# Kernel optimization log

Measured on AMD Instinct MI355X. Metric: run time of the kernel, lower is better.

Reference implementation:

```python
import jax, jax.numpy as jnp
import numpy as np

N, D, H = 50000, 128, 2        # nodes, hidden_size(=ffn_size=out_channels), heads
E = 800000                      # edges
C = D                           # per-head out_channels (PyG TransformerConv)
EPS = 1e-5

def layer_norm(x, g, b):
    mu = jnp.mean(x, axis=-1, keepdims=True)
    var = jnp.mean((x - mu) ** 2, axis=-1, keepdims=True)
    return (x - mu) / jnp.sqrt(var + EPS) * g + b

def setup_inputs() -> dict:
    key = jax.random.key(0)
    ks = jax.random.split(key, 16)
    s_in = 1.0 / np.sqrt(D)
    s_ffn = 1.0 / np.sqrt(D)
    return {
        "x": jax.random.normal(ks[0], (N, D), jnp.float32),
        "edge_index": jax.random.randint(ks[1], (2, E), 0, N, jnp.int64),
        "ln1_g": jnp.ones((D,), jnp.float32),
        "ln1_b": jnp.zeros((D,), jnp.float32),
        "Wq": jax.random.normal(ks[2], (D, H * C), jnp.float32) * s_in,
        "bq": jnp.zeros((H * C,), jnp.float32),
        "Wk": jax.random.normal(ks[3], (D, H * C), jnp.float32) * s_in,
        "bk": jnp.zeros((H * C,), jnp.float32),
        "Wv": jax.random.normal(ks[4], (D, H * C), jnp.float32) * s_in,
        "bv": jnp.zeros((H * C,), jnp.float32),
        "Wskip": jax.random.normal(ks[5], (D, C), jnp.float32) * s_in,
        "bskip": jnp.zeros((C,), jnp.float32),
        "ln2_g": jnp.ones((D,), jnp.float32),
        "ln2_b": jnp.zeros((D,), jnp.float32),
        "W1": jax.random.normal(ks[6], (D, D), jnp.float32) * s_ffn,
        "b1": jnp.zeros((D,), jnp.float32),
        "W2": jax.random.normal(ks[7], (D, D), jnp.float32) * s_ffn,
        "b2": jnp.zeros((D,), jnp.float32),
    }

def reference(x, edge_index, ln1_g, ln1_b, Wq, bq, Wk, bk, Wv, bv,
              Wskip, bskip, ln2_g, ln2_b, W1, b1, W2, b2):
    src, dst = edge_index[0], edge_index[1]  # messages flow src(j) -> dst(i)
    n = x.shape[0]

    # --- self-attention block (pre-norm) ---
    y = layer_norm(x, ln1_g, ln1_b)
    q = (y @ Wq + bq).reshape(n, H, C)
    k = (y @ Wk + bk).reshape(n, H, C)
    v = (y @ Wv + bv).reshape(n, H, C)

    # per-edge attention logits [E, H]
    alpha = jnp.einsum('ehc,ehc->eh', q[dst], k[src]) / jnp.sqrt(jnp.float32(C))
    # softmax over incoming edges of each dst node
    m = jax.ops.segment_max(alpha, dst, num_segments=n)          # [N, H]
    p = jnp.exp(alpha - m[dst])                                  # [E, H]
    denom = jax.ops.segment_sum(p, dst, num_segments=n)          # [N, H]
    a = p / denom[dst]                                           # [E, H]

    attn = jax.ops.segment_sum(a[:, :, None] * v[src], dst, num_segments=n)  # [N,H,C]
    out = attn.mean(axis=1) + (y @ Wskip + bskip)  # concat=False mean + root skip
    x = x + out  # residual (dropout is identity at eval)

    # --- FFN block (pre-norm) ---
    h = layer_norm(x, ln2_g, ln2_b)
    h = jax.nn.gelu(h @ W1 + b1, approximate=False) @ W2 + b2
    return x + h
```

## Files before the change

### kernel.cpp

```cpp
#include <hip/hip_runtime.h>
#include <hip/hip_bf16.h>
#include <math.h>


typedef unsigned short u16;
using short8 = __attribute__((ext_vector_type(8))) short;
using f32x4  = __attribute__((ext_vector_type(4))) float;
using f32x2  = __attribute__((ext_vector_type(2))) float;
using u32x4  = __attribute__((ext_vector_type(4))) unsigned int;

#define EST 64

__device__ __forceinline__ float bf2f(u16 u) {
    return __uint_as_float(((unsigned int)u) << 16);
}
__device__ __forceinline__ u16 f2bf(float f) {
    __hip_bfloat16 h = __float2bfloat16(f);
    return __builtin_bit_cast(u16, h);
}
__device__ __forceinline__ float bfe(short8 v, int j) {
    return bf2f((u16)v[j]);
}
__device__ __forceinline__ void fp8x4_to_f32(int w, float* out) {
    f32x2 lo = __builtin_amdgcn_cvt_pk_f32_fp8(w, false);
    f32x2 hi = __builtin_amdgcn_cvt_pk_f32_fp8(w, true);
    out[0] = lo[0]; out[1] = lo[1]; out[2] = hi[0]; out[3] = hi[1];
}
__device__ __forceinline__ unsigned pack_fp8x4(float4 f) {
    unsigned w = 0;
    w = (unsigned)__builtin_amdgcn_cvt_pk_fp8_f32(f.x, f.y, (int)w, false);
    w = (unsigned)__builtin_amdgcn_cvt_pk_fp8_f32(f.z, f.w, (int)w, true);
    return w;
}

__global__ __launch_bounds__(256) void fused_prep_ln(
    const float* __restrict__ x, const float* __restrict__ ln1g,
    const float* __restrict__ ln1b,
    const float* __restrict__ Wq, const float* __restrict__ Wk,
    const float* __restrict__ Wv, const float* __restrict__ Ws,
    const float* __restrict__ W1, const float* __restrict__ W2,
    const float* __restrict__ bq, const float* __restrict__ bk,
    const float* __restrict__ bv, const float* __restrict__ bs,
    u16* __restrict__ wt, float* __restrict__ bc,
    u16* __restrict__ y, int n)
{
    int gsz = gridDim.x * 256;
    int gtid = blockIdx.x * 256 + threadIdx.x;

    for (int i = gtid; i < 147456 + 896; i += gsz) {
        if (i < 147456) {
            const float* W; int N; int base;
            if      (i <  32768) { W = Wq; N = 256; base = 0; }
            else if (i <  65536) { W = Wk; N = 256; base = 32768; }
            else if (i <  98304) { W = Wv; N = 256; base = 65536; }
            else if (i < 114688) { W = Ws; N = 128; base = 98304; }
            else if (i < 131072) { W = W1; N = 128; base = 114688; }
            else                 { W = W2; N = 128; base = 131072; }
            int j = i - base;
            int nIdx = j >> 7, k = j & 127;
            wt[i] = f2bf(W[(size_t)k * N + nIdx]);
        } else {
            int j = i - 147456;
            float v;
            if      (j < 256) v = bq[j];
            else if (j < 512) v = bk[j - 256];
            else if (j < 768) v = bv[j - 512];
            else              v = bs[j - 768];
            bc[j] = v;
        }
    }
    int lane = threadIdx.x & 63;
    int gw = gtid >> 6, nw = gsz >> 6;
    for (int row = gw; row < n; row += nw) {
        size_t base = (size_t)row * 128;
        float v0 = x[base + lane];
        float v1 = x[base + 64 + lane];
        float s1 = v0 + v1, s2 = v0 * v0 + v1 * v1;
        for (int o = 1; o <= 32; o <<= 1) {
            s1 += __shfl_xor(s1, o);
            s2 += __shfl_xor(s2, o);
        }
        float mu = s1 * (1.f / 128.f);
        float var = s2 * (1.f / 128.f) - mu * mu;
        float rstd = rsqrtf(var + 1e-5f);
        y[base + lane]      = f2bf((v0 - mu) * rstd * ln1g[lane] + ln1b[lane]);
        y[base + 64 + lane] = f2bf((v1 - mu) * rstd * ln1g[64 + lane] + ln1b[64 + lane]);
    }
}

__global__ __launch_bounds__(256, 6) void qkv_gemm(
    const u16* __restrict__ A, const u16* __restrict__ Bt,
    const float* __restrict__ bias, u16* __restrict__ qbuf,
    unsigned char* __restrict__ kv,
    float* __restrict__ skip, int n,
    const int* __restrict__ edst, const int* __restrict__ esrcIn,
    int* __restrict__ cnt, u16* __restrict__ ebuk, int e, int scatBlocks)
{
    __shared__ float epi[4][32 * 33];
    __shared__ uint2 kst[4][2][32][4];
    if (blockIdx.x < (unsigned)scatBlocks) {
        int stride = scatBlocks * 256;
        for (int i = blockIdx.x * 256 + threadIdx.x; i < e; i += stride) {
            int d = edst[i];
            int r = atomicAdd(&cnt[d], 1);
            if (r < EST) ebuk[(size_t)d * EST + r] = (u16)esrcIn[i];
        }
        return;
    }
    int bid = blockIdx.x - scatBlocks;
    int wc = threadIdx.x >> 6, lane = threadIdx.x & 63;
    int r0 = bid * 32;
    int lm = lane & 15, quad = lane >> 4;

    int ar0 = r0 + lm;       if (ar0 > n - 1) ar0 = n - 1;
    int ar1 = r0 + 16 + lm;  if (ar1 > n - 1) ar1 = n - 1;
    const u16* aB0 = A + (size_t)ar0 * 128 + quad * 8;
    const u16* aB1 = A + (size_t)ar1 * 128 + quad * 8;
    short8 a0_0 = *(const short8*)(aB0 + 0);
    short8 a0_1 = *(const short8*)(aB0 + 32);
    short8 a0_2 = *(const short8*)(aB0 + 64);
    short8 a0_3 = *(const short8*)(aB0 + 96);
    short8 a1_0 = *(const short8*)(aB1 + 0);
    short8 a1_1 = *(const short8*)(aB1 + 32);
    short8 a1_2 = *(const short8*)(aB1 + 64);
    short8 a1_3 = *(const short8*)(aB1 + 96);
    asm volatile("" : "+v"(a0_0), "+v"(a0_1), "+v"(a0_2), "+v"(a0_3),
                      "+v"(a1_0), "+v"(a1_1), "+v"(a1_2), "+v"(a1_3));

    float* ep = epi[wc];

    for (int by = 0; by < 7; ++by) {
        int c0 = by * 128;
        const u16* bBase = Bt + (size_t)(c0 + wc * 32 + lm) * 128 + quad * 8;
        f32x4 acc[2][2] = {};
#pragma unroll
        for (int kx = 0; kx < 4; ++kx) {
            short8 a0 = (kx == 0) ? a0_0 : (kx == 1) ? a0_1 : (kx == 2) ? a0_2 : a0_3;
            short8 a1 = (kx == 0) ? a1_0 : (kx == 1) ? a1_1 : (kx == 2) ? a1_2 : a1_3;
#pragma unroll
            for (int j = 0; j < 2; ++j) {
                short8 bj = *(const short8*)(bBase + (size_t)j * 16 * 128 + kx * 32);
                acc[0][j] = __builtin_amdgcn_mfma_f32_16x16x32_bf16(a0, bj, acc[0][j], 0, 0, 0);
                acc[1][j] = __builtin_amdgcn_mfma_f32_16x16x32_bf16(a1, bj, acc[1][j], 0, 0, 0);
            }
        }
#pragma unroll
        for (int j = 0; j < 2; ++j) {
            float bv = bias[c0 + wc * 32 + j * 16 + lm];
#pragma unroll
            for (int rt = 0; rt < 2; ++rt)
#pragma unroll
                for (int i2 = 0; i2 < 4; ++i2)
                    ep[(rt * 16 + quad * 4 + i2) * 33 + j * 16 + lm]
                        = acc[rt][j][i2] + bv;
        }
        if (c0 < 256) {
            int chq = lane & 3;
#pragma unroll
            for (int it = 0; it < 2; ++it) {
                int row = it * 16 + (lane >> 2);
                int gRow = r0 + row;
                if (gRow < n) {
                    const float* ws = ep + row * 33 + chq * 8;
                    short8 o;
#pragma unroll
                    for (int jj = 0; jj < 8; ++jj) o[jj] = (short)f2bf(ws[jj]);
                    *(short8*)(qbuf + (size_t)gRow * 256 + c0 + wc * 32 + chq * 8) = o;
                }
            }
        } else if (c0 < 512) {
            int h = (c0 - 256) >> 7;
            int gp = lane & 3;
#pragma unroll
            for (int it = 0; it < 2; ++it) {
                int row = it * 16 + (lane >> 2);
                const float* ws = ep + row * 33 + gp * 8;
                uint2 kp;
                kp.x = pack_fp8x4(make_float4(ws[0], ws[1], ws[2], ws[3]));
                kp.y = pack_fp8x4(make_float4(ws[4], ws[5], ws[6], ws[7]));
                kst[wc][h][row][gp] = kp;
            }
        } else if (c0 < 768) {
            int h = (c0 - 512) >> 7;
            int gp = lane & 3;
#pragma unroll
            for (int it = 0; it < 2; ++it) {
                int row = it * 16 + (lane >> 2);
                int gRow = r0 + row;
                if (gRow < n) {
                    const float* ws = ep + row * 33 + gp * 8;
                    uint2 kp = kst[wc][h][row][gp];
                    uint4 o;
                    o.x = kp.x;
                    o.y = kp.y;
                    o.z = pack_fp8x4(make_float4(ws[0], ws[1], ws[2], ws[3]));
                    o.w = pack_fp8x4(make_float4(ws[4], ws[5], ws[6], ws[7]));
                    *(uint4*)(kv + (size_t)gRow * 512 + h * 256 + (wc * 4 + gp) * 16) = o;
                }
            }
        } else {
            int chs = lane & 7;
#pragma unroll
            for (int it = 0; it < 4; ++it) {
                int row = it * 8 + (lane >> 3);
                int gRow = r0 + row;
                if (gRow < n) {
                    const float* ws = ep + row * 33 + chs * 4;
                    *(float4*)(skip + (size_t)gRow * 128 + wc * 32 + chs * 4)
                        = make_float4(ws[0], ws[1], ws[2], ws[3]);
                }
            }
        }
    }
}

__global__ __launch_bounds__(256) void attn_kernel(
    const u16* __restrict__ qbuf, const unsigned char* __restrict__ kv,
    const int* __restrict__ cnt,
    const u16* __restrict__ ebuk, const float* __restrict__ x,
    float* __restrict__ sx, const float* __restrict__ g2,
    const float* __restrict__ b2, u16* __restrict__ y, int n, int nwaves)
{
    int wid = threadIdx.x >> 6, lane = threadIdx.x & 63;
    int gw = blockIdx.x * 4 + wid;
    int slot = lane >> 5;
    int sub  = lane & 15;
    int head = (lane >> 4) & 1;
    int colOff = head * 128 + sub * 8;
    int kvOff  = head * 256 + sub * 16;
    const float scale = 0.08838834764831845f;

    for (int i = gw; i < n; i += nwaves) {
        short8 q8 = *(const short8*)(qbuf + (size_t)i * 256 + colOff);
        float qf[8];
#pragma unroll
        for (int j = 0; j < 8; ++j) qf[j] = bfe(q8, j) * scale;

        int deg = cnt[i]; if (deg > EST) deg = EST;
        int beg = i * EST, end = beg + deg;
        float l = 0.f;
        float acc[8] = {};

        int t = beg + slot;
        for (; t + 14 < end; t += 16) {
            int ss[8];
#pragma unroll
            for (int m = 0; m < 8; ++m) ss[m] = (int)ebuk[t + 2 * m];
            u32x4 k0 = *(const u32x4*)(kv + (size_t)ss[0] * 512 + kvOff);
            u32x4 k1 = *(const u32x4*)(kv + (size_t)ss[1] * 512 + kvOff);
            u32x4 k2 = *(const u32x4*)(kv + (size_t)ss[2] * 512 + kvOff);
            u32x4 k3 = *(const u32x4*)(kv + (size_t)ss[3] * 512 + kvOff);
            u32x4 k4 = *(const u32x4*)(kv + (size_t)ss[4] * 512 + kvOff);
            u32x4 k5 = *(const u32x4*)(kv + (size_t)ss[5] * 512 + kvOff);
            u32x4 k6 = *(const u32x4*)(kv + (size_t)ss[6] * 512 + kvOff);
            u32x4 k7 = *(const u32x4*)(kv + (size_t)ss[7] * 512 + kvOff);
            asm volatile("" : "+v"(k0), "+v"(k1), "+v"(k2), "+v"(k3),
                              "+v"(k4), "+v"(k5), "+v"(k6), "+v"(k7));
            u32x4 kvv[8] = {k0, k1, k2, k3, k4, k5, k6, k7};
            float d[8];
#pragma unroll
            for (int m = 0; m < 8; ++m) {
                float kf[8];
                fp8x4_to_f32((int)kvv[m][0], kf);
                fp8x4_to_f32((int)kvv[m][1], kf + 4);
                float dm = 0.f;
#pragma unroll
                for (int j = 0; j < 8; ++j) dm += qf[j] * kf[j];
                d[m] = dm;
            }
#pragma unroll
            for (int o = 1; o <= 8; o <<= 1)
#pragma unroll
                for (int m = 0; m < 8; ++m) d[m] += __shfl_xor(d[m], o);
            float wv[8];
#pragma unroll
            for (int m = 0; m < 8; ++m) { wv[m] = __expf(d[m]); l += wv[m]; }
#pragma unroll
            for (int m = 0; m < 8; ++m) {
                float vf[8];
                fp8x4_to_f32((int)kvv[m][2], vf);
                fp8x4_to_f32((int)kvv[m][3], vf + 4);
#pragma unroll
                for (int j = 0; j < 8; ++j) acc[j] += wv[m] * vf[j];
            }
        }
        for (; t + 6 < end; t += 8) {
            int s0 = (int)ebuk[t],     s1 = (int)ebuk[t + 2];
            int s2 = (int)ebuk[t + 4], s3 = (int)ebuk[t + 6];
            u32x4 kv0 = *(const u32x4*)(kv + (size_t)s0 * 512 + kvOff);
            u32x4 kv1 = *(const u32x4*)(kv + (size_t)s1 * 512 + kvOff);
            u32x4 kv2 = *(const u32x4*)(kv + (size_t)s2 * 512 + kvOff);
            u32x4 kv3 = *(const u32x4*)(kv + (size_t)s3 * 512 + kvOff);
            asm volatile("" : "+v"(kv0), "+v"(kv1), "+v"(kv2), "+v"(kv3));
            float k0f[8], k1f[8], k2f[8], k3f[8];
            float v0f[8], v1f[8], v2f[8], v3f[8];
            fp8x4_to_f32((int)kv0[0], k0f); fp8x4_to_f32((int)kv0[1], k0f + 4);
            fp8x4_to_f32((int)kv1[0], k1f); fp8x4_to_f32((int)kv1[1], k1f + 4);
            fp8x4_to_f32((int)kv2[0], k2f); fp8x4_to_f32((int)kv2[1], k2f + 4);
            fp8x4_to_f32((int)kv3[0], k3f); fp8x4_to_f32((int)kv3[1], k3f + 4);
            fp8x4_to_f32((int)kv0[2], v0f); fp8x4_to_f32((int)kv0[3], v0f + 4);
            fp8x4_to_f32((int)kv1[2], v1f); fp8x4_to_f32((int)kv1[3], v1f + 4);
            fp8x4_to_f32((int)kv2[2], v2f); fp8x4_to_f32((int)kv2[3], v2f + 4);
            fp8x4_to_f32((int)kv3[2], v3f); fp8x4_to_f32((int)kv3[3], v3f + 4);
            float d0 = 0.f, d1 = 0.f, d2 = 0.f, d3 = 0.f;
#pragma unroll
            for (int j = 0; j < 8; ++j) {
                d0 += qf[j] * k0f[j];
                d1 += qf[j] * k1f[j];
                d2 += qf[j] * k2f[j];
                d3 += qf[j] * k3f[j];
            }
#pragma unroll
            for (int o = 1; o <= 8; o <<= 1) {
                d0 += __shfl_xor(d0, o);
                d1 += __shfl_xor(d1, o);
                d2 += __shfl_xor(d2, o);
                d3 += __shfl_xor(d3, o);
            }
            float w0 = __expf(d0), w1 = __expf(d1);
            float w2 = __expf(d2), w3 = __expf(d3);
            l += w0 + w1 + w2 + w3;
#pragma unroll
            for (int j = 0; j < 8; ++j)
                acc[j] += w0 * v0f[j] + w1 * v1f[j] + w2 * v2f[j] + w3 * v3f[j];
        }
        for (; t < end; t += 2) {
            int s0 = (int)ebuk[t];
            u32x4 kv0 = *(const u32x4*)(kv + (size_t)s0 * 512 + kvOff);
            float k0f[8], v0f[8];
            fp8x4_to_f32((int)kv0[0], k0f); fp8x4_to_f32((int)kv0[1], k0f + 4);
            fp8x4_to_f32((int)kv0[2], v0f); fp8x4_to_f32((int)kv0[3], v0f + 4);
            float d0 = 0.f;
#pragma unroll
            for (int j = 0; j < 8; ++j) d0 += qf[j] * k0f[j];
#pragma unroll
            for (int o = 1; o <= 8; o <<= 1) d0 += __shfl_xor(d0, o);
            float w0 = __expf(d0);
            l += w0;
#pragma unroll
            for (int j = 0; j < 8; ++j) acc[j] += w0 * v0f[j];
        }

        float lm2 = l + __shfl_xor(l, 32);
        float inv = (lm2 > 0.f) ? (1.f / lm2) : 0.f;
        float r[8];
#pragma unroll
        for (int j = 0; j < 8; ++j) {
            float a2 = (acc[j] + __shfl_xor(acc[j], 32)) * inv;
            r[j] = 0.5f * (a2 + __shfl_xor(a2, 16));
        }

        if (lane < 16) {
            size_t base = (size_t)i * 128 + sub * 8;
            float4 xv0 = *(const float4*)(x + base);
            float4 xv1 = *(const float4*)(x + base + 4);
            float4 sk0 = *(const float4*)(sx + base);
            float4 sk1 = *(const float4*)(sx + base + 4);
            r[0] += xv0.x + sk0.x; r[1] += xv0.y + sk0.y;
            r[2] += xv0.z + sk0.z; r[3] += xv0.w + sk0.w;
            r[4] += xv1.x + sk1.x; r[5] += xv1.y + sk1.y;
            r[6] += xv1.z + sk1.z; r[7] += xv1.w + sk1.w;
            *(float4*)(sx + base)     = make_float4(r[0], r[1], r[2], r[3]);
            *(float4*)(sx + base + 4) = make_float4(r[4], r[5], r[6], r[7]);
            float s1 = 0.f, s2 = 0.f;
#pragma unroll
            for (int j = 0; j < 8; ++j) { s1 += r[j]; s2 += r[j] * r[j]; }
#pragma unroll
            for (int o = 1; o <= 8; o <<= 1) {
                s1 += __shfl_xor(s1, o);
                s2 += __shfl_xor(s2, o);
            }
            float mu = s1 * (1.f / 128.f);
            float var = s2 * (1.f / 128.f) - mu * mu;
            float rstd = rsqrtf(var + 1e-5f);
            short8 o8;
#pragma unroll
            for (int j = 0; j < 8; ++j)
                o8[j] = (short)f2bf((r[j] - mu) * rstd * g2[sub * 8 + j] + b2[sub * 8 + j]);
            *(short8*)(y + base) = o8;
        }
    }
}

__global__ __launch_bounds__(256, 6) void ffn_kernel(
    const u16* __restrict__ y2, const u16* __restrict__ W1T,
    const float* __restrict__ b1, const u16* __restrict__ W2T,
    const float* __restrict__ b2, const float* __restrict__ x2,
    float* __restrict__ out, int n)
{
    __shared__ u16 t1[32][136];
    int wc = threadIdx.x >> 6, lane = threadIdx.x & 63;
    int lm = lane & 15, quad = lane >> 4;
    int r0 = blockIdx.x * 32;

    int ar0 = r0 + lm;       if (ar0 > n - 1) ar0 = n - 1;
    int ar1 = r0 + 16 + lm;  if (ar1 > n - 1) ar1 = n - 1;
    const u16* aB0 = y2 + (size_t)ar0 * 128 + quad * 8;
    const u16* aB1 = y2 + (size_t)ar1 * 128 + quad * 8;
    short8 a0_0 = *(const short8*)(aB0 + 0);
    short8 a0_1 = *(const short8*)(aB0 + 32);
    short8 a0_2 = *(const short8*)(aB0 + 64);
    short8 a0_3 = *(const short8*)(aB0 + 96);
    short8 a1_0 = *(const short8*)(aB1 + 0);
    short8 a1_1 = *(const short8*)(aB1 + 32);
    short8 a1_2 = *(const short8*)(aB1 + 64);
    short8 a1_3 = *(const short8*)(aB1 + 96);
    asm volatile("" : "+v"(a0_0), "+v"(a0_1), "+v"(a0_2), "+v"(a0_3),
                      "+v"(a1_0), "+v"(a1_1), "+v"(a1_2), "+v"(a1_3));

    f32x4 acc[2][2] = {};
    {
        const u16* bBase = W1T + (size_t)(wc * 32 + lm) * 128 + quad * 8;
#pragma unroll
        for (int kx = 0; kx < 4; ++kx) {
            short8 a0 = (kx == 0) ? a0_0 : (kx == 1) ? a0_1 : (kx == 2) ? a0_2 : a0_3;
            short8 a1 = (kx == 0) ? a1_0 : (kx == 1) ? a1_1 : (kx == 2) ? a1_2 : a1_3;
#pragma unroll
            for (int j = 0; j < 2; ++j) {
                short8 bj = *(const short8*)(bBase + (size_t)j * 16 * 128 + kx * 32);
                acc[0][j] = __builtin_amdgcn_mfma_f32_16x16x32_bf16(a0, bj, acc[0][j], 0, 0, 0);
                acc[1][j] = __builtin_amdgcn_mfma_f32_16x16x32_bf16(a1, bj, acc[1][j], 0, 0, 0);
            }
        }
    }
#pragma unroll
    for (int j = 0; j < 2; ++j) {
        int col = wc * 32 + j * 16 + lm;
        float bv = b1[col];
#pragma unroll
        for (int rt = 0; rt < 2; ++rt)
#pragma unroll
            for (int i2 = 0; i2 < 4; ++i2) {
                float v = acc[rt][j][i2] + bv;
                v = 0.5f * v * (1.f + erff(v * 0.70710678118654752f));
                t1[rt * 16 + quad * 4 + i2][col] = f2bf(v);
            }
    }
    __syncthreads();

    short8 c0_0 = *(const short8*)&t1[lm]     [quad * 8 + 0];
    short8 c0_1 = *(const short8*)&t1[lm]     [quad * 8 + 32];
    short8 c0_2 = *(const short8*)&t1[lm]     [quad * 8 + 64];
    short8 c0_3 = *(const short8*)&t1[lm]     [quad * 8 + 96];
    short8 c1_0 = *(const short8*)&t1[16 + lm][quad * 8 + 0];
    short8 c1_1 = *(const short8*)&t1[16 + lm][quad * 8 + 32];
    short8 c1_2 = *(const short8*)&t1[16 + lm][quad * 8 + 64];
    short8 c1_3 = *(const short8*)&t1[16 + lm][quad * 8 + 96];
    asm volatile("" : "+v"(c0_0), "+v"(c0_1), "+v"(c0_2), "+v"(c0_3),
                      "+v"(c1_0), "+v"(c1_1), "+v"(c1_2), "+v"(c1_3));

    f32x4 acc2[2][2] = {};
    {
        const u16* bBase = W2T + (size_t)(wc * 32 + lm) * 128 + quad * 8;
#pragma unroll
        for (int kx = 0; kx < 4; ++kx) {
            short8 a0 = (kx == 0) ? c0_0 : (kx == 1) ? c0_1 : (kx == 2) ? c0_2 : c0_3;
            short8 a1 = (kx == 0) ? c1_0 : (kx == 1) ? c1_1 : (kx == 2) ? c1_2 : c1_3;
#pragma unroll
            for (int j = 0; j < 2; ++j) {
                short8 bj = *(const short8*)(bBase + (size_t)j * 16 * 128 + kx * 32);
                acc2[0][j] = __builtin_amdgcn_mfma_f32_16x16x32_bf16(a0, bj, acc2[0][j], 0, 0, 0);
                acc2[1][j] = __builtin_amdgcn_mfma_f32_16x16x32_bf16(a1, bj, acc2[1][j], 0, 0, 0);
            }
        }
    }
#pragma unroll
    for (int j = 0; j < 2; ++j) {
        int col = wc * 32 + j * 16 + lm;
        float bv = b2[col];
#pragma unroll
        for (int rt = 0; rt < 2; ++rt)
#pragma unroll
            for (int i2 = 0; i2 < 4; ++i2) {
                int row = r0 + rt * 16 + quad * 4 + i2;
                if (row >= n) continue;
                size_t ob = (size_t)row * 128 + col;
                out[ob] = acc2[rt][j][i2] + bv + x2[ob];
            }
    }
}

extern "C" void kernel_launch(void* const* d_in, const int* in_sizes, int n_in,
                              void* d_out, int out_size, void* d_ws, size_t ws_size,
                              hipStream_t stream)
{
    const float* x    = (const float*)d_in[0];
    const int*   ei   = (const int*)d_in[1];

    int n = in_sizes[0] / 128;
    int e = in_sizes[1] / 2;
    const int* src  = ei;
    const int* dstp = ei + e;

    char* w = (char*)d_ws;
    size_t off = 0;
    auto alloc = [&](size_t bytes) -> void* {
        void* p = w + off;
        off = (off + bytes + 255) & ~(size_t)255;
        return p;
    };
    u16*   y    = (u16*)alloc((size_t)n * 128 * 2);
    u16*   qbuf = (u16*)alloc((size_t)n * 256 * 2);
    unsigned char* kvb = (unsigned char*)alloc((size_t)n * 512);
    float* sx   = (float*)alloc((size_t)n * 128 * 4);
    u16*   wt   = (u16*)alloc((size_t)147456 * 2);
    float* bc   = (float*)alloc(896 * 4);
    int* cnt    = (int*)alloc((size_t)n * 4);
    u16* ebuk   = (u16*)alloc((size_t)n * EST * 2);

    int gr32 = (n + 31) / 32;
    int scatBlocks = 1024;
    int attnBlocks = 2048;

    hipMemsetAsync(cnt, 0, (size_t)n * sizeof(int), stream);
    fused_prep_ln<<<2048, 256, 0, stream>>>(
        x, (const float*)d_in[2], (const float*)d_in[3],
        (const float*)d_in[4], (const float*)d_in[6], (const float*)d_in[8],
        (const float*)d_in[10], (const float*)d_in[14], (const float*)d_in[16],
        (const float*)d_in[5], (const float*)d_in[7], (const float*)d_in[9],
        (const float*)d_in[11], wt, bc, y, n);
    qkv_gemm<<<scatBlocks + gr32, 256, 0, stream>>>(
        y, wt, bc, qbuf, kvb, sx, n, dstp, src, cnt, ebuk, e, scatBlocks);
    attn_kernel<<<attnBlocks, 256, 0, stream>>>(qbuf, kvb, cnt, ebuk, x, sx,
                                                (const float*)d_in[12],
                                                (const float*)d_in[13], y, n,
                                                attnBlocks * 4);
    ffn_kernel<<<gr32, 256, 0, stream>>>(y, wt + 114688, (const float*)d_in[15],
                                         wt + 131072, (const float*)d_in[17],
                                         sx, (float*)d_out, n);
}
```

Baseline: 334.8 us.

## Two-pass edge bucketing via coarse 64-node bins with LDS atomics

Replaces the single-pass global-atomic scatter of edges into per-node buckets with a two-stage scheme. The first stage runs inside the prep kernel and bins edges into coarse 64-node bins with packed (src, local dst) words. The second stage runs inside the GEMM kernel, where each block uses shared-memory atomics to fill the per-node buckets and write the counts. This cuts contention on global atomics and gives more local writes, at the cost of an extra pass over an intermediate buffer and a per-bin capacity cap (BCAP) that could drop edges if a bin overflows.

```diff
diff --git a/kernel.cpp b/kernel.cpp
--- a/kernel.cpp
+++ b/kernel.cpp
@@ -10,6 +10,7 @@
 using u32x4  = __attribute__((ext_vector_type(4))) unsigned int;
 
 #define EST 64
+#define BCAP 2048
 
 __device__ __forceinline__ float bf2f(u16 u) {
     return __uint_as_float(((unsigned int)u) << 16);
@@ -42,10 +43,24 @@
     const float* __restrict__ bq, const float* __restrict__ bk,
     const float* __restrict__ bv, const float* __restrict__ bs,
     u16* __restrict__ wt, float* __restrict__ bc,
-    u16* __restrict__ y, int n)
+    u16* __restrict__ y, int n,
+    const int* __restrict__ edst, const int* __restrict__ esrcIn,
+    unsigned* __restrict__ ebin, int* __restrict__ bcnt, int e, int binBlocks)
 {
-    int gsz = gridDim.x * 256;
-    int gtid = blockIdx.x * 256 + threadIdx.x;
+    if (blockIdx.x < (unsigned)binBlocks) {
+        int stride = binBlocks * 256;
+        for (int i = blockIdx.x * 256 + threadIdx.x; i < e; i += stride) {
+            int d = edst[i];
+            int b = d >> 6;
+            int r = atomicAdd(&bcnt[b], 1);
+            if (r < BCAP)
+                ebin[(size_t)b * BCAP + r] =
+                    ((unsigned)esrcIn[i] << 6) | (unsigned)(d & 63);
+        }
+        return;
+    }
+    int gsz = (gridDim.x - binBlocks) * 256;
+    int gtid = (blockIdx.x - binBlocks) * 256 + threadIdx.x;
 
     for (int i = gtid; i < 147456 + 896; i += gsz) {
         if (i < 147456) {
@@ -93,21 +108,31 @@
     const float* __restrict__ bias, u16* __restrict__ qbuf,
     unsigned char* __restrict__ kv,
     float* __restrict__ skip, int n,
-    const int* __restrict__ edst, const int* __restrict__ esrcIn,
-    int* __restrict__ cnt, u16* __restrict__ ebuk, int e, int scatBlocks)
+    const unsigned* __restrict__ ebin, const int* __restrict__ bcnt,
+    int* __restrict__ cnt, u16* __restrict__ ebuk, int nbins)
 {
     __shared__ float epi[4][32 * 33];
     __shared__ uint2 kst[4][2][32][4];
-    if (blockIdx.x < (unsigned)scatBlocks) {
-        int stride = scatBlocks * 256;
-        for (int i = blockIdx.x * 256 + threadIdx.x; i < e; i += stride) {
-            int d = edst[i];
-            int r = atomicAdd(&cnt[d], 1);
-            if (r < EST) ebuk[(size_t)d * EST + r] = (u16)esrcIn[i];
-        }
+    __shared__ int lcnt[64];
+    if (blockIdx.x < (unsigned)nbins) {
+        int b = blockIdx.x;
+        if (threadIdx.x < 64) lcnt[threadIdx.x] = 0;
+        __syncthreads();
+        int cb = bcnt[b]; if (cb > BCAP) cb = BCAP;
+        for (int i = threadIdx.x; i < cb; i += 256) {
+            unsigned p = ebin[(size_t)b * BCAP + i];
+            int dl = (int)(p & 63u);
+            int s  = (int)(p >> 6);
+            int r = atomicAdd(&lcnt[dl], 1);
+            if (r < EST)
+                ebuk[((size_t)(b * 64 + dl)) * EST + r] = (u16)s;
+        }
+        __syncthreads();
+        int node = b * 64 + threadIdx.x;
+        if (threadIdx.x < 64 && node < n) cnt[node] = lcnt[threadIdx.x];
         return;
     }
-    int bid = blockIdx.x - scatBlocks;
+    int bid = blockIdx.x - nbins;
     int wc = threadIdx.x >> 6, lane = threadIdx.x & 63;
     int r0 = bid * 32;
     int lm = lane & 15, quad = lane >> 4;
@@ -507,20 +532,23 @@
     float* bc   = (float*)alloc(896 * 4);
     int* cnt    = (int*)alloc((size_t)n * 4);
     u16* ebuk   = (u16*)alloc((size_t)n * EST * 2);
+    int nbins   = (n + 63) / 64;
+    unsigned* ebin = (unsigned*)alloc((size_t)nbins * BCAP * 4);
+    int* bcnt   = (int*)alloc((size_t)nbins * 4);
 
     int gr32 = (n + 31) / 32;
-    int scatBlocks = 1024;
+    int binBlocks = 512;
     int attnBlocks = 2048;
 
-    hipMemsetAsync(cnt, 0, (size_t)n * sizeof(int), stream);
-    fused_prep_ln<<<2048, 256, 0, stream>>>(
+    hipMemsetAsync(bcnt, 0, (size_t)nbins * sizeof(int), stream);
+    fused_prep_ln<<<2048 + binBlocks, 256, 0, stream>>>(
         x, (const float*)d_in[2], (const float*)d_in[3],
         (const float*)d_in[4], (const float*)d_in[6], (const float*)d_in[8],
         (const float*)d_in[10], (const float*)d_in[14], (const float*)d_in[16],
         (const float*)d_in[5], (const float*)d_in[7], (const float*)d_in[9],
-        (const float*)d_in[11], wt, bc, y, n);
-    qkv_gemm<<<scatBlocks + gr32, 256, 0, stream>>>(
-        y, wt, bc, qbuf, kvb, sx, n, dstp, src, cnt, ebuk, e, scatBlocks);
+        (const float*)d_in[11], wt, bc, y, n, dstp, src, ebin, bcnt, e, binBlocks);
+    qkv_gemm<<<nbins + gr32, 256, 0, stream>>>(
+        y, wt, bc, qbuf, kvb, sx, n, ebin, bcnt, cnt, ebuk, nbins);
     attn_kernel<<<attnBlocks, 256, 0, stream>>>(qbuf, kvb, cnt, ebuk, x, sx,
                                                 (const float*)d_in[12],
                                                 (const float*)d_in[13], y, n,
```

Result: slower. 473.1 us (+41.3%).
